# Kernel tuning notes

Measured on AMD Instinct MI355X. Metric: run time of the kernel, lower is better.

Reference implementation:

```python
import jax, jax.numpy as jnp
import numpy as np

B, S, D = 8, 4096, 256


def setup_inputs() -> dict:
    key = jax.random.key(0)
    kq, kk, kv, kb = jax.random.split(key, 4)
    q = jax.random.normal(kq, (B, S, D), dtype=jnp.float32)
    k = jax.random.normal(kk, (B, S, D), dtype=jnp.float32)
    v = jax.random.normal(kv, (B, S, D), dtype=jnp.float32)
    beta = jax.random.uniform(kb, (B, S), dtype=jnp.float32)
    return {"q": q, "k": k, "v": v, "beta": beta}


def reference(q, k, v, beta):
    # Delta-rule linear attention recurrence:
    #   h_t = beta_t * h_{t-1} + k_t^T v_t   (h: [B, D, D])
    #   o_t = q_t @ h_t                      (o: [B, D])
    dtype = q.dtype
    b, s, d = q.shape
    h0 = jnp.zeros((b, d, d), dtype=dtype)

    def step(h, inp):
        q_t, k_t, v_t, b_t = inp  # q_t/k_t/v_t: [B, D], b_t: [B]
        h = h * b_t[:, None, None] + jnp.einsum('bi,bj->bij', k_t, v_t)
        o_t = jnp.einsum('bi,bij->bj', q_t, h)
        return h, o_t

    xs = (q.transpose(1, 0, 2), k.transpose(1, 0, 2),
          v.transpose(1, 0, 2), beta.T)  # time-major
    _, out = jax.lax.scan(step, h0, xs)  # out: [S, B, D]
    return out.transpose(1, 0, 2)  # [B, S, D]
```

## Files before the change

### kernel.cpp

```cpp
#include <hip/hip_runtime.h>
#include <hip/hip_bf16.h>
#include <math.h>


#define B_ 8
#define S_ 4096
#define D_ 256
#define L_ 128
#define C_ (S_ / L_)
#define BC_ (B_ * C_)

typedef __attribute__((ext_vector_type(8))) short s8v;
typedef __attribute__((ext_vector_type(4))) float f4v;
typedef unsigned short u16;
typedef unsigned int u32;

__device__ __forceinline__ u32 pk2(float lo, float hi) {
  union { __hip_bfloat162 h; u32 u; } cv;
  cv.h = __float22bfloat162_rn(make_float2(lo, hi));
  return cv.u;
}
__device__ __forceinline__ s8v pack8(const float4 a, const float4 b) {
  union { u32 u[4]; s8v v; } r;
  r.u[0] = pk2(a.x, a.y); r.u[1] = pk2(a.z, a.w);
  r.u[2] = pk2(b.x, b.y); r.u[3] = pk2(b.z, b.w);
  return r.v;
}

__device__ __forceinline__ void beta_scan128(const float* betap, float* ls,
                                             int tid) {
  if (tid < 64) {
    float x = log2f(fmaxf(betap[tid], 1e-30f));
#pragma unroll
    for (int off = 1; off < 64; off <<= 1) {
      float y = __shfl_up(x, off);
      if (tid >= off) x += y;
    }
    ls[tid] = x;
    const float tot0 = __shfl(x, 63);
    float z = log2f(fmaxf(betap[64 + tid], 1e-30f));
#pragma unroll
    for (int off = 1; off < 64; off <<= 1) {
      float y = __shfl_up(z, off);
      if (tid >= off) z += y;
    }
    ls[64 + tid] = z + tot0;
  }
}

__global__ __launch_bounds__(1024, 1) void ks_summary8(
    const float* __restrict__ kg, const float* __restrict__ vg,
    const float* __restrict__ beta, u16* __restrict__ A,
    float* __restrict__ P)
{
  __shared__ float ls[L_];
  __shared__ __align__(16) u16 U[2][256 * 66];
  __shared__ __align__(16) u16 BN[64 * 264];

  const int bc = blockIdx.x;
  const int b = bc / C_, c = bc % C_;
  const int tid = threadIdx.x;
  const float* betap = beta + (size_t)b * S_ + (size_t)c * L_;
  const float* kbase = kg + ((size_t)b * S_ + (size_t)c * L_) * D_;
  const float* vbase = vg + ((size_t)b * S_ + (size_t)c * L_) * D_;

  beta_scan128(betap, ls, tid);
  __syncthreads();
  const float ltot = ls[L_ - 1];
  if (tid == 0) P[bc] = exp2f(ltot);

  const int hh = tid >> 9;
  const int t2 = tid & 511;
  const int iLs = t2 & 15;
  const int sps = t2 >> 4;
  const int s0s = sps * 2;
  const int sg = hh * 64 + s0s;

  {
    const float* src0 = kbase + (size_t)sg * D_;
    const float* src1 = src0 + D_;
    const float w0 = exp2f(ltot - ls[sg]);
    const float w1 = exp2f(ltot - ls[sg + 1]);
    u16* dst = U[hh];
#pragma unroll
    for (int p = 0; p < 4; ++p) {
      const int i0 = p * 64 + iLs * 4;
      float a0[4], a1[4];
      *(float4*)a0 = *(const float4*)(src0 + i0);
      *(float4*)a1 = *(const float4*)(src1 + i0);
#pragma unroll
      for (int u = 0; u < 4; ++u)
        *(u32*)&dst[(i0 + u) * 66 + s0s] = pk2(a0[u] * w0, a1[u] * w1);
    }
  }
  __syncthreads();

  const int lane = tid & 63, wave = tid >> 6;
  const int quad = lane >> 4, l15 = lane & 15;
  const int i0w = wave * 16;

  s8v af[4];
#pragma unroll
  for (int ks = 0; ks < 4; ++ks)
    af[ks] = *(const s8v*)&U[ks >> 1][(i0w + l15) * 66 +
                                      (ks & 1) * 32 + quad * 8];
  __syncthreads();

  {
    const float* src0 = vbase + (size_t)sg * D_;
    const float* src1 = src0 + D_;
    u16* dst = U[hh];
#pragma unroll
    for (int p = 0; p < 4; ++p) {
      const int i0 = p * 64 + iLs * 4;
      float a0[4], a1[4];
      *(float4*)a0 = *(const float4*)(src0 + i0);
      *(float4*)a1 = *(const float4*)(src1 + i0);
#pragma unroll
      for (int u = 0; u < 4; ++u)
        *(u32*)&dst[(i0 + u) * 66 + s0s] = pk2(a0[u], a1[u]);
    }
  }
  __syncthreads();

  u16* Ab = A + (size_t)bc * D_ * D_;

  for (int ng = 0; ng < 4; ++ng) {
    f4v acc[4];
#pragma unroll
    for (int nt = 0; nt < 4; ++nt) acc[nt] = (f4v){0.f, 0.f, 0.f, 0.f};

#pragma unroll
    for (int ks = 0; ks < 4; ++ks) {
      const int so = (ks & 1) * 32 + quad * 8;
      s8v bv[4];
#pragma unroll
      for (int nt = 0; nt < 4; ++nt)
        bv[nt] = *(const s8v*)&U[ks >> 1][(ng * 64 + nt * 16 + l15) * 66 + so];
#pragma unroll
      for (int nt = 0; nt < 4; ++nt)
        acc[nt] = __builtin_amdgcn_mfma_f32_16x16x32_bf16(
            af[ks], bv[nt], acc[nt], 0, 0, 0);
    }
#pragma unroll
    for (int nt = 0; nt < 4; ++nt) {
      const int jl = nt * 16 + l15;
      uint2 w;
      w.x = pk2(acc[nt][0], acc[nt][1]);
      w.y = pk2(acc[nt][2], acc[nt][3]);
      *(uint2*)&BN[jl * 264 + i0w + quad * 4] = w;
    }
    __syncthreads();
    {
      const int jl = tid >> 4;
      const int il = (tid & 15) * 8;
#pragma unroll
      for (int p = 0; p < 2; ++p) {
        const int iu = il + p * 128;
        *(s8v*)&Ab[(size_t)(ng * 64 + jl) * D_ + iu] =
            *(const s8v*)&BN[jl * 264 + iu];
      }
    }
    __syncthreads();
  }
}

__global__ __launch_bounds__(256) void ks_scan8(
    u16* __restrict__ A, const float* __restrict__ P)
{
  const int g = blockIdx.x;
  const int b = g >> 6;
  const int unit = ((g & 63) << 8) + threadIdx.x;
  u16* base = A + (size_t)b * ((size_t)C_ * D_ * D_) + (size_t)unit * 4;
  const float* Pb = P + b * C_;

  uint2 d[C_];
#pragma unroll
  for (int c = 0; c < C_; ++c)
    d[c] = *(const uint2*)(base + (size_t)c * (D_ * D_));

  float h0 = 0.f, h1 = 0.f, h2 = 0.f, h3 = 0.f;
#pragma unroll
  for (int c = 0; c < C_; ++c) {
    const float pc = Pb[c];
    const uint2 u = d[c];
    const float a0 = __uint_as_float(u.x << 16);
    const float a1 = __uint_as_float(u.x & 0xFFFF0000u);
    const float a2 = __uint_as_float(u.y << 16);
    const float a3 = __uint_as_float(u.y & 0xFFFF0000u);
    d[c].x = pk2(h0, h1);
    d[c].y = pk2(h2, h3);
    h0 = fmaf(pc, h0, a0); h1 = fmaf(pc, h1, a1);
    h2 = fmaf(pc, h2, a2); h3 = fmaf(pc, h3, a3);
  }
#pragma unroll
  for (int c = 0; c < C_; ++c)
    *(uint2*)(base + (size_t)c * (D_ * D_)) = d[c];
}

__global__ __launch_bounds__(1024, 1) void ks_output8(
    const float* __restrict__ qg, const float* __restrict__ kg,
    const float* __restrict__ vg, const float* __restrict__ beta,
    const u16* __restrict__ Hg, float* __restrict__ outg)
{
  __shared__ float ls[L_];
  __shared__ float cv[L_];
  __shared__ __align__(16) u16 QB[L_ * 264];
  __shared__ __align__(16) u16 Tm[L_ * 136];
  __shared__ __align__(16) u16 VT[256 * 66];

  const int bc = blockIdx.x;
  const int b = bc / C_, c = bc % C_;
  const int tid = threadIdx.x;
  const float* betap = beta + (size_t)b * S_ + (size_t)c * L_;
  const float* qbase = qg + ((size_t)b * S_ + (size_t)c * L_) * D_;
  const float* kbase = kg + ((size_t)b * S_ + (size_t)c * L_) * D_;
  const float* vbase = vg + ((size_t)b * S_ + (size_t)c * L_) * D_;
  const u16* Hb = Hg + (size_t)bc * D_ * D_;

  beta_scan128(betap, ls, tid);

  {
    const int t = tid >> 3;
    const int d8 = (tid & 7) * 8;
    const float* src = qbase + (size_t)t * D_;
#pragma unroll
    for (int p = 0; p < 4; ++p) {
      const int d0 = d8 + p * 64;
      const s8v pk = pack8(*(const float4*)(src + d0),
                           *(const float4*)(src + d0 + 4));
      *(s8v*)&QB[t * 264 + d0] = pk;
    }
  }
  __syncthreads();
  if (tid < L_) cv[tid] = exp2f(ls[tid]);

  const int lane = tid & 63, wave = tid >> 6;
  const int quad = lane >> 4, l15 = lane & 15;
  const int j0w = wave * 16;

  {
    const int mA = (wave & 7) * 16;
    const int tg = (wave >> 3) * 64;
    f4v accA[4];
#pragma unroll
    for (int i = 0; i < 4; ++i) accA[i] = (f4v){0.f, 0.f, 0.f, 0.f};
#pragma unroll
    for (int kd = 0; kd < 8; ++kd) {
      const int d0 = kd * 32 + quad * 8;
      const float* krow = kbase + (size_t)(mA + l15) * D_ + d0;
      const s8v afr = pack8(*(const float4*)krow, *(const float4*)(krow + 4));
#pragma unroll
      for (int nt = 0; nt < 4; ++nt) {
        const s8v bf = *(const s8v*)&QB[(tg + nt * 16 + l15) * 264 + d0];
        accA[nt] = __builtin_amdgcn_mfma_f32_16x16x32_bf16(afr, bf, accA[nt],
                                                           0, 0, 0);
      }
    }
#pragma unroll
    for (int nt = 0; nt < 4; ++nt) {
      const int t = tg + nt * 16 + l15;
      const float lt = ls[t];
      const int s0 = mA + quad * 4;
      float v[4];
#pragma unroll
      for (int r = 0; r < 4; ++r) {
        const int s = s0 + r;
        v[r] = (s <= t) ? accA[nt][r] * exp2f(lt - ls[s]) : 0.f;
      }
      uint2 w;
      w.x = pk2(v[0], v[1]);
      w.y = pk2(v[2], v[3]);
      *(uint2*)&Tm[t * 136 + s0] = w;
    }
  }

  {
    const int jL = tid & 15;
    const int sp = (tid >> 4) & 31;
    const int hb = tid >> 9;
    const int s0 = sp * 2;
    const float* src0 = vbase + (size_t)s0 * D_ + hb * 128;
    const float* src1 = src0 + D_;
#pragma unroll
    for (int p = 0; p < 2; ++p) {
      const int j0 = hb * 128 + p * 64 + jL * 4;
      float a0[4], a1[4];
      *(float4*)a0 = *(const float4*)(src0 + p * 64 + jL * 4);
      *(float4*)a1 = *(const float4*)(src1 + p * 64 + jL * 4);
#pragma unroll
      for (int u = 0; u < 4; ++u)
        *(u32*)&VT[(j0 + u) * 66 + s0] = pk2(a0[u], a1[u]);
    }
  }

  s8v hc = *(const s8v*)(Hb + (size_t)(j0w + l15) * D_ + quad * 8);

  __syncthreads();

  f4v acc[8];
#pragma unroll
  for (int nt = 0; nt < 8; ++nt) acc[nt] = (f4v){0.f, 0.f, 0.f, 0.f};

#pragma unroll
  for (int ks = 0; ks < 8; ++ks) {
    const int io = ks * 32 + quad * 8;
    s8v hn = hc;
    if (ks < 7)
      hn = *(const s8v*)(Hb + (size_t)(j0w + l15) * D_ + io + 32);
    s8v bf[8];
#pragma unroll
    for (int nt = 0; nt < 8; ++nt)
      bf[nt] = *(const s8v*)&QB[(nt * 16 + l15) * 264 + io];
#pragma unroll
    for (int nt = 0; nt < 8; ++nt)
      acc[nt] = __builtin_amdgcn_mfma_f32_16x16x32_bf16(hc, bf[nt], acc[nt],
                                                        0, 0, 0);
    hc = hn;
  }
#pragma unroll
  for (int nt = 0; nt < 8; ++nt) {
    const float ct = cv[nt * 16 + l15];
    acc[nt][0] *= ct; acc[nt][1] *= ct;
    acc[nt][2] *= ct; acc[nt][3] *= ct;
  }

#pragma unroll
  for (int ks = 0; ks < 2; ++ks) {
    const int so = ks * 32 + quad * 8;
    const s8v afv = *(const s8v*)&VT[(j0w + l15) * 66 + so];
    s8v bf[8];
#pragma unroll
    for (int nt = 0; nt < 8; ++nt)
      bf[nt] = *(const s8v*)&Tm[(nt * 16 + l15) * 136 + so];
#pragma unroll
    for (int nt = 0; nt < 8; ++nt)
      acc[nt] = __builtin_amdgcn_mfma_f32_16x16x32_bf16(afv, bf[nt], acc[nt],
                                                        0, 0, 0);
  }

  __syncthreads();
  {
    const int jL = tid & 15;
    const int sp = (tid >> 4) & 31;
    const int hb = tid >> 9;
    const int s0 = sp * 2;
    const float* src0 = vbase + (size_t)(64 + s0) * D_ + hb * 128;
    const float* src1 = src0 + D_;
#pragma unroll
    for (int p = 0; p < 2; ++p) {
      const int j0 = hb * 128 + p * 64 + jL * 4;
      float a0[4], a1[4];
      *(float4*)a0 = *(const float4*)(src0 + p * 64 + jL * 4);
      *(float4*)a1 = *(const float4*)(src1 + p * 64 + jL * 4);
#pragma unroll
      for (int u = 0; u < 4; ++u)
        *(u32*)&VT[(j0 + u) * 66 + s0] = pk2(a0[u], a1[u]);
    }
  }
  __syncthreads();
#pragma unroll
  for (int ks = 0; ks < 2; ++ks) {
    const int so = ks * 32 + quad * 8;
    const s8v afv = *(const s8v*)&VT[(j0w + l15) * 66 + so];
    s8v bf[8];
#pragma unroll
    for (int nt = 0; nt < 8; ++nt)
      bf[nt] = *(const s8v*)&Tm[(nt * 16 + l15) * 136 + 64 + so];
#pragma unroll
    for (int nt = 0; nt < 8; ++nt)
      acc[nt] = __builtin_amdgcn_mfma_f32_16x16x32_bf16(afv, bf[nt], acc[nt],
                                                        0, 0, 0);
  }

  float* ob = outg + ((size_t)b * S_ + (size_t)c * L_) * D_;
#pragma unroll
  for (int nt = 0; nt < 8; ++nt) {
    const int t = nt * 16 + l15;
    const int j0 = j0w + quad * 4;
    float4 o;
    o.x = acc[nt][0]; o.y = acc[nt][1];
    o.z = acc[nt][2]; o.w = acc[nt][3];
    *(float4*)(ob + (size_t)t * D_ + j0) = o;
  }
}

extern "C" void kernel_launch(void* const* d_in, const int* in_sizes, int n_in,
                              void* d_out, int out_size, void* d_ws,
                              size_t ws_size, hipStream_t stream) {
  const float* q = (const float*)d_in[0];
  const float* k = (const float*)d_in[1];
  const float* v = (const float*)d_in[2];
  const float* beta = (const float*)d_in[3];
  float* out = (float*)d_out;

  u16* A = (u16*)d_ws;
  float* P = (float*)((char*)d_ws + (size_t)BC_ * D_ * D_ * sizeof(u16));

  ks_summary8<<<dim3(BC_), dim3(1024), 0, stream>>>(k, v, beta, A, P);
  ks_scan8<<<dim3(512), dim3(256), 0, stream>>>(A, P);
  ks_output8<<<dim3(BC_), dim3(1024), 0, stream>>>(q, k, v, beta, A, out);
}
```

Before: 179.0 us.

## Emit transposed bf16 V from summary kernel and reuse in output kernel

```diff
diff --git a/kernel.cpp b/kernel.cpp
--- a/kernel.cpp
+++ b/kernel.cpp
@@ -48,10 +48,10 @@
   }
 }
 
-__global__ __launch_bounds__(1024, 1) void ks_summary8(
+__global__ __launch_bounds__(1024, 1) void ks_front9(
     const float* __restrict__ kg, const float* __restrict__ vg,
     const float* __restrict__ beta, u16* __restrict__ A,
-    float* __restrict__ P)
+    float* __restrict__ P, u16* __restrict__ Vt)
 {
   __shared__ float ls[L_];
   __shared__ __align__(16) u16 U[2][256 * 66];
@@ -72,8 +72,7 @@
   const int hh = tid >> 9;
   const int t2 = tid & 511;
   const int iLs = t2 & 15;
-  const int sps = t2 >> 4;
-  const int s0s = sps * 2;
+  const int s0s = (t2 >> 4) * 2;
   const int sg = hh * 64 + s0s;
 
   {
@@ -122,6 +121,17 @@
     }
   }
   __syncthreads();
+
+  {
+    u16* Vtb = Vt + (size_t)bc * (D_ * L_);
+    const int j = tid >> 2;
+    const int qq = tid & 3;
+    const u16* srcl = &U[qq >> 1][j * 66 + (qq & 1) * 32];
+    u16* dst = Vtb + (size_t)j * L_ + qq * 32;
+#pragma unroll
+    for (int p = 0; p < 4; ++p)
+      *(s8v*)(dst + p * 8) = *(const s8v*)(srcl + p * 8);
+  }
 
   u16* Ab = A + (size_t)bc * D_ * D_;
 
@@ -165,7 +175,7 @@
   }
 }
 
-__global__ __launch_bounds__(256) void ks_scan8(
+__global__ __launch_bounds__(256) void ks_scan9(
     u16* __restrict__ A, const float* __restrict__ P)
 {
   const int g = blockIdx.x;
@@ -198,16 +208,15 @@
     *(uint2*)(base + (size_t)c * (D_ * D_)) = d[c];
 }
 
-__global__ __launch_bounds__(1024, 1) void ks_output8(
+__global__ __launch_bounds__(1024, 1) void ks_output9(
     const float* __restrict__ qg, const float* __restrict__ kg,
-    const float* __restrict__ vg, const float* __restrict__ beta,
-    const u16* __restrict__ Hg, float* __restrict__ outg)
+    const float* __restrict__ beta, const u16* __restrict__ Hg,
+    const u16* __restrict__ Vt, float* __restrict__ outg)
 {
   __shared__ float ls[L_];
   __shared__ float cv[L_];
   __shared__ __align__(16) u16 QB[L_ * 264];
   __shared__ __align__(16) u16 Tm[L_ * 136];
-  __shared__ __align__(16) u16 VT[256 * 66];
 
   const int bc = blockIdx.x;
   const int b = bc / C_, c = bc % C_;
@@ -215,8 +224,8 @@
   const float* betap = beta + (size_t)b * S_ + (size_t)c * L_;
   const float* qbase = qg + ((size_t)b * S_ + (size_t)c * L_) * D_;
   const float* kbase = kg + ((size_t)b * S_ + (size_t)c * L_) * D_;
-  const float* vbase = vg + ((size_t)b * S_ + (size_t)c * L_) * D_;
   const u16* Hb = Hg + (size_t)bc * D_ * D_;
+  const u16* Vtb = Vt + (size_t)bc * (D_ * L_);
 
   beta_scan128(betap, ls, tid);
 
@@ -232,12 +241,21 @@
       *(s8v*)&QB[t * 264 + d0] = pk;
     }
   }
-  __syncthreads();
-  if (tid < L_) cv[tid] = exp2f(ls[tid]);
 
   const int lane = tid & 63, wave = tid >> 6;
   const int quad = lane >> 4, l15 = lane & 15;
   const int j0w = wave * 16;
+
+  s8v hfr[8], vfr[4];
+#pragma unroll
+  for (int ks = 0; ks < 8; ++ks)
+    hfr[ks] = *(const s8v*)(Hb + (size_t)(j0w + l15) * D_ + ks * 32 + quad * 8);
+#pragma unroll
+  for (int ks = 0; ks < 4; ++ks)
+    vfr[ks] = *(const s8v*)(Vtb + (size_t)(j0w + l15) * L_ + ks * 32 + quad * 8);
+
+  __syncthreads();
+  if (tid < L_) cv[tid] = exp2f(ls[tid]);
 
   {
     const int mA = (wave & 7) * 16;
@@ -274,28 +292,6 @@
       *(uint2*)&Tm[t * 136 + s0] = w;
     }
   }
-
-  {
-    const int jL = tid & 15;
-    const int sp = (tid >> 4) & 31;
-    const int hb = tid >> 9;
-    const int s0 = sp * 2;
-    const float* src0 = vbase + (size_t)s0 * D_ + hb * 128;
-    const float* src1 = src0 + D_;
-#pragma unroll
-    for (int p = 0; p < 2; ++p) {
-      const int j0 = hb * 128 + p * 64 + jL * 4;
-      float a0[4], a1[4];
-      *(float4*)a0 = *(const float4*)(src0 + p * 64 + jL * 4);
-      *(float4*)a1 = *(const float4*)(src1 + p * 64 + jL * 4);
-#pragma unroll
-      for (int u = 0; u < 4; ++u)
-        *(u32*)&VT[(j0 + u) * 66 + s0] = pk2(a0[u], a1[u]);
-    }
-  }
-
-  s8v hc = *(const s8v*)(Hb + (size_t)(j0w + l15) * D_ + quad * 8);
-
   __syncthreads();
 
   f4v acc[8];
@@ -305,18 +301,14 @@
 #pragma unroll
   for (int ks = 0; ks < 8; ++ks) {
     const int io = ks * 32 + quad * 8;
-    s8v hn = hc;
-    if (ks < 7)
-      hn = *(const s8v*)(Hb + (size_t)(j0w + l15) * D_ + io + 32);
     s8v bf[8];
 #pragma unroll
     for (int nt = 0; nt < 8; ++nt)
       bf[nt] = *(const s8v*)&QB[(nt * 16 + l15) * 264 + io];
 #pragma unroll
     for (int nt = 0; nt < 8; ++nt)
-      acc[nt] = __builtin_amdgcn_mfma_f32_16x16x32_bf16(hc, bf[nt], acc[nt],
-                                                        0, 0, 0);
-    hc = hn;
+      acc[nt] = __builtin_amdgcn_mfma_f32_16x16x32_bf16(hfr[ks], bf[nt],
+                                                        acc[nt], 0, 0, 0);
   }
 #pragma unroll
   for (int nt = 0; nt < 8; ++nt) {
@@ -326,51 +318,16 @@
   }
 
 #pragma unroll
-  for (int ks = 0; ks < 2; ++ks) {
+  for (int ks = 0; ks < 4; ++ks) {
     const int so = ks * 32 + quad * 8;
-    const s8v afv = *(const s8v*)&VT[(j0w + l15) * 66 + so];
     s8v bf[8];
 #pragma unroll
     for (int nt = 0; nt < 8; ++nt)
       bf[nt] = *(const s8v*)&Tm[(nt * 16 + l15) * 136 + so];
 #pragma unroll
     for (int nt = 0; nt < 8; ++nt)
-      acc[nt] = __builtin_amdgcn_mfma_f32_16x16x32_bf16(afv, bf[nt], acc[nt],
-                                                        0, 0, 0);
-  }
-
-  __syncthreads();
-  {
-    const int jL = tid & 15;
-    const int sp = (tid >> 4) & 31;
-    const int hb = tid >> 9;
-    const int s0 = sp * 2;
-    const float* src0 = vbase + (size_t)(64 + s0) * D_ + hb * 128;
-    const float* src1 = src0 + D_;
-#pragma unroll
-    for (int p = 0; p < 2; ++p) {
-      const int j0 = hb * 128 + p * 64 + jL * 4;
-      float a0[4], a1[4];
-      *(float4*)a0 = *(const float4*)(src0 + p * 64 + jL * 4);
-      *(float4*)a1 = *(const float4*)(src1 + p * 64 + jL * 4);
-#pragma unroll
-      for (int u = 0; u < 4; ++u)
-        *(u32*)&VT[(j0 + u) * 66 + s0] = pk2(a0[u], a1[u]);
-    }
-  }
-  __syncthreads();
-#pragma unroll
-  for (int ks = 0; ks < 2; ++ks) {
-    const int so = ks * 32 + quad * 8;
-    const s8v afv = *(const s8v*)&VT[(j0w + l15) * 66 + so];
-    s8v bf[8];
-#pragma unroll
-    for (int nt = 0; nt < 8; ++nt)
-      bf[nt] = *(const s8v*)&Tm[(nt * 16 + l15) * 136 + 64 + so];
-#pragma unroll
-    for (int nt = 0; nt < 8; ++nt)
-      acc[nt] = __builtin_amdgcn_mfma_f32_16x16x32_bf16(afv, bf[nt], acc[nt],
-                                                        0, 0, 0);
+      acc[nt] = __builtin_amdgcn_mfma_f32_16x16x32_bf16(vfr[ks], bf[nt],
+                                                        acc[nt], 0, 0, 0);
   }
 
   float* ob = outg + ((size_t)b * S_ + (size_t)c * L_) * D_;
@@ -395,9 +352,10 @@
   float* out = (float*)d_out;
 
   u16* A = (u16*)d_ws;
-  float* P = (float*)((char*)d_ws + (size_t)BC_ * D_ * D_ * sizeof(u16));
-
-  ks_summary8<<<dim3(BC_), dim3(1024), 0, stream>>>(k, v, beta, A, P);
-  ks_scan8<<<dim3(512), dim3(256), 0, stream>>>(A, P);
-  ks_output8<<<dim3(BC_), dim3(1024), 0, stream>>>(q, k, v, beta, A, out);
-}
+  float* P = (float*)((char*)d_ws + 33554432);
+  u16* Vt = (u16*)((char*)d_ws + 33554432 + 1024);
+
+  ks_front9<<<dim3(BC_), dim3(1024), 0, stream>>>(k, v, beta, A, P, Vt);
+  ks_scan9<<<dim3(512), dim3(256), 0, stream>>>(A, P);
+  ks_output9<<<dim3(BC_), dim3(1024), 0, stream>>>(q, k, beta, A, Vt, out);
+}
```

Measured after the change: 188.3 us. 5.2% more time.
